# Performance work log

Hardware: AMD Instinct MI355X
Metric: run time of the kernel (lower is better)

Reference implementation:

```python
import jax, jax.numpy as jnp
import numpy as np

B, T, C, D = 64, 4096, 51, 64
MASK_PROB = 0.3
LN_EPS = 1e-5


def setup_inputs() -> dict:
    key = jax.random.key(0)
    k0, k1, k2, k3, k4 = jax.random.split(key, 5)
    x = jax.random.normal(k0, (B, T, C), dtype=jnp.float32)
    # xavier_uniform_ then *= 0.5 (as in reset_parameters)
    bound = float(np.sqrt(6.0 / (C + D)))
    W = jax.random.uniform(k1, (C, D), jnp.float32, -bound, bound) * 0.5
    Wm = jax.random.uniform(k2, (C, D), jnp.float32, -bound, bound) * 0.5
    gamma = jnp.ones((D,), jnp.float32)
    beta = jnp.zeros((D,), jnp.float32)
    time_mask = jax.random.bernoulli(k3, MASK_PROB, (B, T))
    sensor_mask = jax.random.bernoulli(k4, MASK_PROB, (B, C))
    return {"x": x, "W": W, "Wm": Wm, "gamma": gamma, "beta": beta,
            "time_mask": time_mask, "sensor_mask": sensor_mask}


def reference(x, W, Wm, gamma, beta, time_mask, sensor_mask):
    # mask[b,t,c] = time_mask[b,t] OR sensor_mask[b,c]
    mask = (time_mask[:, :, None] | sensor_mask[:, None, :]).astype(x.dtype)  # [B,T,C]
    # Fused masked reductions (math-equivalent to the broadcast [B,T,C,D] path)
    xu = jnp.einsum('btc,cd->btd', x * (1.0 - mask), W)   # [B,T,D]
    xm = jnp.einsum('btc,cd->btd', mask, Wm)              # [B,T,D]
    out = xu + xm
    # LayerNorm over last dim
    mu = jnp.mean(out, axis=-1, keepdims=True)
    var = jnp.mean((out - mu) ** 2, axis=-1, keepdims=True)
    out = (out - mu) * jax.lax.rsqrt(var + LN_EPS) * gamma + beta
    return out
```

## Files before the change

kernel.cpp:

```cpp
#include <hip/hip_runtime.h>

#define BB 64
#define TT 4096
#define CC 51
#define DD 64
#define LN_EPS 1e-5f

typedef __attribute__((ext_vector_type(8))) short short8;
typedef __attribute__((ext_vector_type(4))) float f32x4;

union FragU { int i[4]; short8 s; };

#define DPP_QP_1032   0xB1
#define DPP_QP_2301   0x4E
#define DPP_ROW_HMIRR 0x141
#define DPP_ROW_MIRR  0x140

__device__ __forceinline__ float dpp_add(float v, int tag) {
  int t;
  switch (tag) {
    case 0: t = __builtin_amdgcn_update_dpp(0, __float_as_int(v), DPP_QP_1032,   0xF, 0xF, true); break;
    case 1: t = __builtin_amdgcn_update_dpp(0, __float_as_int(v), DPP_QP_2301,   0xF, 0xF, true); break;
    case 2: t = __builtin_amdgcn_update_dpp(0, __float_as_int(v), DPP_ROW_HMIRR, 0xF, 0xF, true); break;
    default: t = __builtin_amdgcn_update_dpp(0, __float_as_int(v), DPP_ROW_MIRR, 0xF, 0xF, true); break;
  }
  return v + __int_as_float(t);
}
__device__ __forceinline__ float allsum16(float v) {
  v = dpp_add(v, 0); v = dpp_add(v, 1); v = dpp_add(v, 2); v = dpp_add(v, 3);
  return v;
}
__device__ __forceinline__ float allsum64(float v) {
  v = allsum16(v);
  v += __shfl_xor(v, 16, 64);
  v += __shfl_xor(v, 32, 64);
  return v;
}

__device__ __forceinline__ int pack_hl(float x) {
  const unsigned u = __float_as_uint(x);
  const unsigned h = u >> 16;
  const float hf = __uint_as_float(u & 0xFFFF0000u);
  const unsigned l = __float_as_uint(x - hf) >> 16;
  return (int)(h | (l << 16));
}

__global__ __launch_bounds__(256, 4)
void ipmask_mfma7(const float* __restrict__ x, const float* __restrict__ W,
                  const float* __restrict__ Wm,
                  const float* __restrict__ gamma, const float* __restrict__ beta,
                  const int* __restrict__ tmask, const int* __restrict__ smask,
                  float* __restrict__ out) {
  const int t = threadIdx.x, L = t & 63, w = t >> 6;
  const int q = L >> 4, m16 = L & 15;
  const int gw = (blockIdx.x << 2) + w;
  const int b = gw >> 7;
  const int rowBase = (b << 12) + ((gw & 127) << 5);

  const int* smB = smask + b * CC;

  __shared__ int tabHL[4][4][64][4];
  __shared__ float red[8][64];

  float xf[2][4][4];
#pragma unroll
  for (int mt = 0; mt < 2; ++mt) {
    const float* xr = x + (size_t)(rowBase + mt * 16 + m16) * CC;
#pragma unroll
    for (int ks = 0; ks < 3; ++ks) {
      f32x4 v;
      __builtin_memcpy(&v, xr + ks * 16 + q * 4, 16);
      xf[mt][ks][0] = v[0]; xf[mt][ks][1] = v[1];
      xf[mt][ks][2] = v[2]; xf[mt][ks][3] = v[3];
    }
    if (q == 0) {
      xf[mt][3][0] = xr[48]; xf[mt][3][1] = xr[49]; xf[mt][3][2] = xr[50];
      xf[mt][3][3] = 0.0f;
    } else {
#pragma unroll
      for (int j = 0; j < 4; ++j) xf[mt][3][j] = 0.0f;
    }
  }
  const int tmv = tmask[rowBase + (L & 31)];

  {
    const int ntb = w, laneb = L;
    const int qb = laneb >> 4, m16b = laneb & 15;
    const int nb = ntb * 16 + m16b;
#pragma unroll
    for (int k = 0; k < 4; ++k) {
      int hl[4];
#pragma unroll
      for (int j = 0; j < 4; ++j) {
        const int c = k * 16 + qb * 4 + j;
        float we = 0.0f;
        if (c < CC) { if (!smB[c]) we = W[c * DD + nb]; }
        const unsigned u = __float_as_uint(we);
        const unsigned h = u >> 16;
        const float hf = __uint_as_float(u & 0xFFFF0000u);
        const unsigned l = __float_as_uint(we - hf) >> 16;
        hl[j] = (int)(h | (l << 16));
      }
      __builtin_memcpy(&tabHL[k][ntb][laneb][0], hl, 16);
    }
  }

  {
    const int c0 = w * 13, c1 = (c0 + 13 < CC) ? c0 + 13 : CC;
    float bs = 0.0f, f = 0.0f;
    for (int c = c0; c < c1; ++c) {
      const float wmv = Wm[c * DD + L];
      const float sf = (float)smB[c];
      bs = fmaf(sf, wmv, bs);
      f += wmv;
    }
    red[w * 2][L] = bs;
    red[w * 2 + 1][L] = f;
  }
  __syncthreads();
  const float gl = gamma[L], bl = beta[L];
  float biasL, consL;
  {
    const float bs = (red[0][L] + red[2][L]) + (red[4][L] + red[6][L]);
    const float f  = (red[1][L] + red[3][L]) + (red[5][L] + red[7][L]);
    biasL = bs;
    const float s1 = allsum64(f);
    const float s2 = allsum64(f * f);
    const float mu = s1 * (1.0f / 64.0f);
    const float vr = fmaf(-mu, mu, s2 * (1.0f / 64.0f));
    const float rs = rsqrtf(vr + LN_EPS);
    consL = fmaf((f - mu) * rs, gl, bl);
  }
  float bias_[4], cons_[4], g_[4], b_[4];
#pragma unroll
  for (int nt = 0; nt < 4; ++nt) {
    const int src = nt * 16 + m16;
    bias_[nt] = __shfl(biasL, src, 64);
    cons_[nt] = __shfl(consL, src, 64);
    g_[nt]    = __shfl(gl, src, 64);
    b_[nt]    = __shfl(bl, src, 64);
  }

  f32x4 acc[2][4];
#pragma unroll
  for (int nt = 0; nt < 4; ++nt) {
#pragma unroll
    for (int mt = 0; mt < 2; ++mt) {
      acc[mt][nt][0] = bias_[nt]; acc[mt][nt][1] = bias_[nt];
      acc[mt][nt][2] = bias_[nt]; acc[mt][nt][3] = bias_[nt];
    }
  }

#pragma unroll
  for (int ks = 0; ks < 4; ++ks) {
    FragU au[2];
#pragma unroll
    for (int mt = 0; mt < 2; ++mt)
#pragma unroll
      for (int j = 0; j < 4; ++j) au[mt].i[j] = pack_hl(xf[mt][ks][j]);
#pragma unroll
    for (int nt = 0; nt < 4; ++nt) {
      int hl[4];
      __builtin_memcpy(hl, &tabHL[ks][nt][L][0], 16);
      FragU bmu, bcu;
#pragma unroll
      for (int j = 0; j < 4; ++j) {
        bmu.i[j] = (hl[j] & 0xFFFF) | (hl[j] << 16);
        bcu.i[j] = (int)((unsigned)hl[j] >> 16);
      }
#pragma unroll
      for (int mt = 0; mt < 2; ++mt) {
        acc[mt][nt] = __builtin_amdgcn_mfma_f32_16x16x32_bf16(au[mt].s, bmu.s, acc[mt][nt], 0, 0, 0);
        acc[mt][nt] = __builtin_amdgcn_mfma_f32_16x16x32_bf16(au[mt].s, bcu.s, acc[mt][nt], 0, 0, 0);
      }
    }
  }

#pragma unroll
  for (int mt = 0; mt < 2; ++mt) {
#pragma unroll
    for (int rg = 0; rg < 4; ++rg) {
      float su = 0.0f, sq = 0.0f;
#pragma unroll
      for (int nt = 0; nt < 4; ++nt) {
        const float v = acc[mt][nt][rg];
        su += v;
        sq = fmaf(v, v, sq);
      }
      su = allsum16(su);
      sq = allsum16(sq);
      const float mu = su * (1.0f / 64.0f);
      const float vr = fmaf(-mu, mu, sq * (1.0f / 64.0f));
      const float rs = rsqrtf(vr + LN_EPS);
      const int rloc = mt * 16 + q * 4 + rg;
      const int tm = __shfl(tmv, rloc, 64);
      const size_t obase = (size_t)(rowBase + rloc) * DD;
#pragma unroll
      for (int nt = 0; nt < 4; ++nt) {
        float val = fmaf((acc[mt][nt][rg] - mu) * rs, g_[nt], b_[nt]);
        if (tm) val = cons_[nt];
        __builtin_nontemporal_store(val, &out[obase + nt * 16 + m16]);
      }
    }
  }
}

extern "C" void kernel_launch(void* const* d_in, const int* in_sizes, int n_in,
                              void* d_out, int out_size, void* d_ws, size_t ws_size,
                              hipStream_t stream) {
  const float* x     = (const float*)d_in[0];
  const float* W     = (const float*)d_in[1];
  const float* Wm    = (const float*)d_in[2];
  const float* gamma = (const float*)d_in[3];
  const float* beta  = (const float*)d_in[4];
  const int*   tmask = (const int*)d_in[5];
  const int*   smask = (const int*)d_in[6];
  float* out = (float*)d_out;

  ipmask_mfma7<<<dim3(2048), dim3(256), 0, stream>>>(
      x, W, Wm, gamma, beta, tmask, smask, out);
}
```

Before: 129.2 us.

## Process 64 rows per wave in pipelined 16-row chunks with vectorized stores

Each wave now handles 64 rows instead of 32, and the grid is halved to 1024 blocks, so the per-block W/Wm table setup is spread over twice as many rows. The rows are processed in four 16-row chunks, with x loads for later chunks issued before the MFMA and LayerNorm of earlier chunks to hide global-memory latency. The output column mapping is permuted (n = m16*4 + nt) so each lane writes a contiguous float4 with one nontemporal vector store. W and Wm loads are hoisted into registers ahead of the smask-dependent packing. The cost is higher register pressure and fewer blocks to spread across CUs.

```diff
diff --git a/kernel.cpp b/kernel.cpp
--- a/kernel.cpp
+++ b/kernel.cpp
@@ -45,80 +45,161 @@
   return (int)(h | (l << 16));
 }
 
+__device__ __forceinline__ void loadX(const float* __restrict__ x,
+                                      const int* __restrict__ tmask,
+                                      int rowCh, int q, int m16, int L,
+                                      float (&xf)[4][4], int& tm) {
+  const float* xr = x + (size_t)(rowCh + m16) * CC;
+#pragma unroll
+  for (int ks = 0; ks < 3; ++ks) {
+    f32x4 v;
+    __builtin_memcpy(&v, xr + ks * 16 + q * 4, 16);
+    xf[ks][0] = v[0]; xf[ks][1] = v[1]; xf[ks][2] = v[2]; xf[ks][3] = v[3];
+  }
+  if (q == 0) {
+    xf[3][0] = xr[48]; xf[3][1] = xr[49]; xf[3][2] = xr[50]; xf[3][3] = 0.0f;
+  } else {
+    xf[3][0] = 0.0f; xf[3][1] = 0.0f; xf[3][2] = 0.0f; xf[3][3] = 0.0f;
+  }
+  tm = tmask[rowCh + (L & 15)];
+}
+
+__device__ __forceinline__ void compMFMA(const int (*tab)[4][64][4],
+                                         const float (&xf)[4][4], int L,
+                                         const float (&bias_)[4],
+                                         f32x4 (&acc)[4]) {
+#pragma unroll
+  for (int nt = 0; nt < 4; ++nt) {
+    acc[nt][0] = bias_[nt]; acc[nt][1] = bias_[nt];
+    acc[nt][2] = bias_[nt]; acc[nt][3] = bias_[nt];
+  }
+#pragma unroll
+  for (int ks = 0; ks < 4; ++ks) {
+    FragU au;
+#pragma unroll
+    for (int j = 0; j < 4; ++j) au.i[j] = pack_hl(xf[ks][j]);
+#pragma unroll
+    for (int nt = 0; nt < 4; ++nt) {
+      int hl[4];
+      __builtin_memcpy(hl, &tab[ks][nt][L][0], 16);
+      FragU bmu, bcu;
+#pragma unroll
+      for (int j = 0; j < 4; ++j) {
+        bmu.i[j] = (hl[j] & 0xFFFF) | (hl[j] << 16);
+        bcu.i[j] = (int)((unsigned)hl[j] >> 16);
+      }
+      acc[nt] = __builtin_amdgcn_mfma_f32_16x16x32_bf16(au.s, bmu.s, acc[nt], 0, 0, 0);
+      acc[nt] = __builtin_amdgcn_mfma_f32_16x16x32_bf16(au.s, bcu.s, acc[nt], 0, 0, 0);
+    }
+  }
+}
+
+__device__ __forceinline__ void lnStore(const f32x4 (&acc)[4], int tmv,
+                                        int q, int m16,
+                                        const float (&cons_)[4],
+                                        const float (&g_)[4], const float (&b_)[4],
+                                        float* __restrict__ outCh) {
+#pragma unroll
+  for (int rg = 0; rg < 4; ++rg) {
+    float su = 0.0f, sq = 0.0f;
+#pragma unroll
+    for (int nt = 0; nt < 4; ++nt) {
+      const float v = acc[nt][rg];
+      su += v;
+      sq = fmaf(v, v, sq);
+    }
+    su = allsum16(su);
+    sq = allsum16(sq);
+    const float mu = su * (1.0f / 64.0f);
+    const float vr = fmaf(-mu, mu, sq * (1.0f / 64.0f));
+    const float rs = rsqrtf(vr + LN_EPS);
+    const int rloc = q * 4 + rg;
+    const int tm = __shfl(tmv, rloc, 64);
+    f32x4 v4;
+#pragma unroll
+    for (int nt = 0; nt < 4; ++nt) {
+      float val = fmaf((acc[nt][rg] - mu) * rs, g_[nt], b_[nt]);
+      if (tm) val = cons_[nt];
+      v4[nt] = val;
+    }
+    __builtin_nontemporal_store(v4, (f32x4*)(outCh + rloc * DD + m16 * 4));
+  }
+}
+
 __global__ __launch_bounds__(256, 4)
-void ipmask_mfma7(const float* __restrict__ x, const float* __restrict__ W,
-                  const float* __restrict__ Wm,
-                  const float* __restrict__ gamma, const float* __restrict__ beta,
-                  const int* __restrict__ tmask, const int* __restrict__ smask,
-                  float* __restrict__ out) {
+void ipmask_mfma12(const float* __restrict__ x, const float* __restrict__ W,
+                   const float* __restrict__ Wm,
+                   const float* __restrict__ gamma, const float* __restrict__ beta,
+                   const int* __restrict__ tmask, const int* __restrict__ smask,
+                   float* __restrict__ out) {
   const int t = threadIdx.x, L = t & 63, w = t >> 6;
   const int q = L >> 4, m16 = L & 15;
   const int gw = (blockIdx.x << 2) + w;
-  const int b = gw >> 7;
-  const int rowBase = (b << 12) + ((gw & 127) << 5);
+  const int b = gw >> 6;
+  const int rowBase = (b << 12) + ((gw & 63) << 6);
 
   const int* smB = smask + b * CC;
 
   __shared__ int tabHL[4][4][64][4];
   __shared__ float red[8][64];
 
-  float xf[2][4][4];
-#pragma unroll
-  for (int mt = 0; mt < 2; ++mt) {
-    const float* xr = x + (size_t)(rowBase + mt * 16 + m16) * CC;
-#pragma unroll
-    for (int ks = 0; ks < 3; ++ks) {
-      f32x4 v;
-      __builtin_memcpy(&v, xr + ks * 16 + q * 4, 16);
-      xf[mt][ks][0] = v[0]; xf[mt][ks][1] = v[1];
-      xf[mt][ks][2] = v[2]; xf[mt][ks][3] = v[3];
-    }
-    if (q == 0) {
-      xf[mt][3][0] = xr[48]; xf[mt][3][1] = xr[49]; xf[mt][3][2] = xr[50];
-      xf[mt][3][3] = 0.0f;
-    } else {
-#pragma unroll
-      for (int j = 0; j < 4; ++j) xf[mt][3][j] = 0.0f;
-    }
-  }
-  const int tmv = tmask[rowBase + (L & 31)];
-
-  {
-    const int ntb = w, laneb = L;
-    const int qb = laneb >> 4, m16b = laneb & 15;
-    const int nb = ntb * 16 + m16b;
+  float wraw[16];
+  {
+    const int nb = m16 * 4 + w;
+#pragma unroll
+    for (int k = 0; k < 4; ++k)
+#pragma unroll
+      for (int j = 0; j < 4; ++j) {
+        const int c = k * 16 + q * 4 + j;
+        wraw[k * 4 + j] = (c < CC) ? W[c * DD + nb] : 0.0f;
+      }
+  }
+  float wmr[13];
+  const int c0 = w * 13;
+#pragma unroll
+  for (int i = 0; i < 13; ++i) {
+    const int c = c0 + i;
+    wmr[i] = (c < CC) ? Wm[c * DD + L] : 0.0f;
+  }
+  const float gl = gamma[L], bl = beta[L];
+
+  float x0[4][4], x1[4][4], x2[4][4];
+  int tm0, tm1, tm2, tm3;
+  loadX(x, tmask, rowBase,      q, m16, L, x0, tm0);
+  loadX(x, tmask, rowBase + 16, q, m16, L, x1, tm1);
+  loadX(x, tmask, rowBase + 32, q, m16, L, x2, tm2);
+
+  {
 #pragma unroll
     for (int k = 0; k < 4; ++k) {
       int hl[4];
 #pragma unroll
       for (int j = 0; j < 4; ++j) {
-        const int c = k * 16 + qb * 4 + j;
-        float we = 0.0f;
-        if (c < CC) { if (!smB[c]) we = W[c * DD + nb]; }
+        const int c = k * 16 + q * 4 + j;
+        const int smv = (c < CC) ? smB[c] : 1;
+        const float we = smv ? 0.0f : wraw[k * 4 + j];
         const unsigned u = __float_as_uint(we);
         const unsigned h = u >> 16;
         const float hf = __uint_as_float(u & 0xFFFF0000u);
         const unsigned l = __float_as_uint(we - hf) >> 16;
         hl[j] = (int)(h | (l << 16));
       }
-      __builtin_memcpy(&tabHL[k][ntb][laneb][0], hl, 16);
-    }
-  }
-
-  {
-    const int c0 = w * 13, c1 = (c0 + 13 < CC) ? c0 + 13 : CC;
+      __builtin_memcpy(&tabHL[k][w][L][0], hl, 16);
+    }
+  }
+  {
     float bs = 0.0f, f = 0.0f;
-    for (int c = c0; c < c1; ++c) {
-      const float wmv = Wm[c * DD + L];
-      const float sf = (float)smB[c];
-      bs = fmaf(sf, wmv, bs);
-      f += wmv;
+#pragma unroll
+    for (int i = 0; i < 13; ++i) {
+      const int c = c0 + i;
+      const float sf = (c < CC) ? (float)smB[c] : 0.0f;
+      bs = fmaf(sf, wmr[i], bs);
+      f += wmr[i];
     }
     red[w * 2][L] = bs;
     red[w * 2 + 1][L] = f;
   }
   __syncthreads();
-  const float gl = gamma[L], bl = beta[L];
   float biasL, consL;
   {
     const float bs = (red[0][L] + red[2][L]) + (red[4][L] + red[6][L]);
@@ -134,75 +215,28 @@
   float bias_[4], cons_[4], g_[4], b_[4];
 #pragma unroll
   for (int nt = 0; nt < 4; ++nt) {
-    const int src = nt * 16 + m16;
+    const int src = m16 * 4 + nt;
     bias_[nt] = __shfl(biasL, src, 64);
     cons_[nt] = __shfl(consL, src, 64);
     g_[nt]    = __shfl(gl, src, 64);
     b_[nt]    = __shfl(bl, src, 64);
   }
 
-  f32x4 acc[2][4];
-#pragma unroll
-  for (int nt = 0; nt < 4; ++nt) {
-#pragma unroll
-    for (int mt = 0; mt < 2; ++mt) {
-      acc[mt][nt][0] = bias_[nt]; acc[mt][nt][1] = bias_[nt];
-      acc[mt][nt][2] = bias_[nt]; acc[mt][nt][3] = bias_[nt];
-    }
-  }
-
-#pragma unroll
-  for (int ks = 0; ks < 4; ++ks) {
-    FragU au[2];
-#pragma unroll
-    for (int mt = 0; mt < 2; ++mt)
-#pragma unroll
-      for (int j = 0; j < 4; ++j) au[mt].i[j] = pack_hl(xf[mt][ks][j]);
-#pragma unroll
-    for (int nt = 0; nt < 4; ++nt) {
-      int hl[4];
-      __builtin_memcpy(hl, &tabHL[ks][nt][L][0], 16);
-      FragU bmu, bcu;
-#pragma unroll
-      for (int j = 0; j < 4; ++j) {
-        bmu.i[j] = (hl[j] & 0xFFFF) | (hl[j] << 16);
-        bcu.i[j] = (int)((unsigned)hl[j] >> 16);
-      }
-#pragma unroll
-      for (int mt = 0; mt < 2; ++mt) {
-        acc[mt][nt] = __builtin_amdgcn_mfma_f32_16x16x32_bf16(au[mt].s, bmu.s, acc[mt][nt], 0, 0, 0);
-        acc[mt][nt] = __builtin_amdgcn_mfma_f32_16x16x32_bf16(au[mt].s, bcu.s, acc[mt][nt], 0, 0, 0);
-      }
-    }
-  }
-
-#pragma unroll
-  for (int mt = 0; mt < 2; ++mt) {
-#pragma unroll
-    for (int rg = 0; rg < 4; ++rg) {
-      float su = 0.0f, sq = 0.0f;
-#pragma unroll
-      for (int nt = 0; nt < 4; ++nt) {
-        const float v = acc[mt][nt][rg];
-        su += v;
-        sq = fmaf(v, v, sq);
-      }
-      su = allsum16(su);
-      sq = allsum16(sq);
-      const float mu = su * (1.0f / 64.0f);
-      const float vr = fmaf(-mu, mu, sq * (1.0f / 64.0f));
-      const float rs = rsqrtf(vr + LN_EPS);
-      const int rloc = mt * 16 + q * 4 + rg;
-      const int tm = __shfl(tmv, rloc, 64);
-      const size_t obase = (size_t)(rowBase + rloc) * DD;
-#pragma unroll
-      for (int nt = 0; nt < 4; ++nt) {
-        float val = fmaf((acc[mt][nt][rg] - mu) * rs, g_[nt], b_[nt]);
-        if (tm) val = cons_[nt];
-        __builtin_nontemporal_store(val, &out[obase + nt * 16 + m16]);
-      }
-    }
-  }
+  float* outW = out + (size_t)rowBase * DD;
+  f32x4 acc[4];
+
+  compMFMA(tabHL, x0, L, bias_, acc);
+  loadX(x, tmask, rowBase + 48, q, m16, L, x0, tm3);
+  lnStore(acc, tm0, q, m16, cons_, g_, b_, outW);
+
+  compMFMA(tabHL, x1, L, bias_, acc);
+  lnStore(acc, tm1, q, m16, cons_, g_, b_, outW + 16 * DD);
+
+  compMFMA(tabHL, x2, L, bias_, acc);
+  lnStore(acc, tm2, q, m16, cons_, g_, b_, outW + 32 * DD);
+
+  compMFMA(tabHL, x0, L, bias_, acc);
+  lnStore(acc, tm3, q, m16, cons_, g_, b_, outW + 48 * DD);
 }
 
 extern "C" void kernel_launch(void* const* d_in, const int* in_sizes, int n_in,
@@ -217,6 +251,6 @@
   const int*   smask = (const int*)d_in[6];
   float* out = (float*)d_out;
 
-  ipmask_mfma7<<<dim3(2048), dim3(256), 0, stream>>>(
+  ipmask_mfma12<<<dim3(1024), dim3(256), 0, stream>>>(
       x, W, Wm, gamma, beta, tmask, smask, out);
 }
```

Measured after the change: 199.1 us. +54.0%, slower.
